# Kernel tuning notes

Hardware: AMD Instinct MI355X
Metric: run time of the kernel (lower is better)

The kernel has to match this reference:

```python
import jax, jax.numpy as jnp
import numpy as np

EMBED_DIM = 1024
N_HEADS = 16
HEAD_DIM = EMBED_DIM // N_HEADS
B, T = 4, 2048


def setup_inputs() -> dict:
    key = jax.random.key(0)
    ks = jax.random.split(key, 5)
    s = 1.0 / np.sqrt(EMBED_DIM)
    return {
        "x": jax.random.normal(ks[0], (B, T, EMBED_DIM), dtype=jnp.float32),
        "w_qkv": jax.random.normal(ks[1], (EMBED_DIM, 3 * EMBED_DIM), dtype=jnp.float32) * s,
        "b_qkv": jnp.zeros((3 * EMBED_DIM,), dtype=jnp.float32),
        "w_out": jax.random.normal(ks[2], (EMBED_DIM, EMBED_DIM), dtype=jnp.float32) * s,
        "b_out": jnp.zeros((EMBED_DIM,), dtype=jnp.float32),
    }


def reference(x, w_qkv, b_qkv, w_out, b_out):
    Bb, Tt, C = x.shape
    qkv = x @ w_qkv + b_qkv                      # (B, T, 3C)
    q, k, v = jnp.split(qkv, 3, axis=-1)
    # (B, H, T, Dh)
    def to_heads(t):
        return t.reshape(Bb, Tt, N_HEADS, HEAD_DIM).transpose(0, 2, 1, 3)
    q, k, v = to_heads(q), to_heads(k), to_heads(v)
    scale = 1.0 / np.sqrt(HEAD_DIM)
    scores = jnp.einsum("bhqd,bhkd->bhqk", q, k) * scale  # (B, H, T, T)
    causal = jnp.tril(jnp.ones((Tt, Tt), dtype=bool))
    scores = jnp.where(causal[None, None], scores, -jnp.inf)
    attn = jax.nn.softmax(scores, axis=-1)
    out = jnp.einsum("bhqk,bhkd->bhqd", attn, v)  # (B, H, T, Dh)
    out = out.transpose(0, 2, 1, 3).reshape(Bb, Tt, C)
    return out @ w_out + b_out
```

## Files before the change

kernel.cpp:

```cpp
#include <hip/hip_runtime.h>

typedef __bf16 bf16;
typedef __bf16 bf16x4 __attribute__((ext_vector_type(4)));
typedef __bf16 bf16x8 __attribute__((ext_vector_type(8)));
typedef float f32x4 __attribute__((ext_vector_type(4)));

#define TSEQ 2048
#define NHEAD 16

__device__ __forceinline__ void gload_lds16(const bf16* g, bf16* s) {
  __builtin_amdgcn_global_load_lds(
      (const __attribute__((address_space(1))) void*)g,
      (__attribute__((address_space(3))) void*)s, 16, 0, 0);
}

__global__ __launch_bounds__(256) void cvt_f32_bf16_kernel(
    const float* __restrict__ in, bf16* __restrict__ out) {
  size_t i = ((size_t)blockIdx.x * 256 + threadIdx.x) * 8;
  float4 v0 = ((const float4*)(in + i))[0];
  float4 v1 = ((const float4*)(in + i))[1];
  bf16x8 o;
  o[0] = (bf16)v0.x; o[1] = (bf16)v0.y; o[2] = (bf16)v0.z; o[3] = (bf16)v0.w;
  o[4] = (bf16)v1.x; o[5] = (bf16)v1.y; o[6] = (bf16)v1.z; o[7] = (bf16)v1.w;
  *(bf16x8*)(out + i) = o;
}

__global__ __launch_bounds__(256) void transpose_cvt_kernel(
    const float* __restrict__ in, bf16* __restrict__ out, int K, int N) {
  __shared__ float tile[32][33];
  int n0 = blockIdx.x * 32, k0 = blockIdx.y * 32;
  int tx = threadIdx.x & 31, ty = threadIdx.x >> 5;
#pragma unroll
  for (int i = ty; i < 32; i += 8)
    tile[i][tx] = in[(size_t)(k0 + i) * N + n0 + tx];
  __syncthreads();
#pragma unroll
  for (int i = ty; i < 32; i += 8)
    out[(size_t)(n0 + i) * K + k0 + tx] = (bf16)tile[tx][i];
}

template <typename OutT>
__global__ __launch_bounds__(256, 2) void gemm_bf16_kernel(
    const bf16* __restrict__ A, const bf16* __restrict__ Bt,
    const float* __restrict__ bias, OutT* __restrict__ C,
    int M, int N, int K, int scale_cols) {
  alignas(16) __shared__ bf16 As[128 * 32];
  alignas(16) __shared__ bf16 Bs[128 * 32];
  const int row0 = blockIdx.y * 128, col0 = blockIdx.x * 128;
  const int tid = threadIdx.x;
  const int wave = tid >> 6, lane = tid & 63;
  const int quad = lane >> 4, lm = lane & 15;
  const int wm = (wave >> 1) * 64, wn = (wave & 1) * 64;

  f32x4 acc[4][4];
  const f32x4 z4 = {0.0f, 0.0f, 0.0f, 0.0f};
#pragma unroll
  for (int i = 0; i < 4; i++)
#pragma unroll
    for (int j = 0; j < 4; j++) acc[i][j] = z4;

  const int sr = tid >> 2, sc = (tid & 3) * 8;
  const bf16* apg = A + (size_t)(row0 + sr) * K + sc;
  const bf16* bpg = Bt + (size_t)(col0 + sr) * K + sc;
  const size_t half = (size_t)64 * K;

  for (int k0 = 0; k0 < K; k0 += 32) {
    __syncthreads();
    gload_lds16(apg, &As[tid * 8]);
    gload_lds16(apg + half, &As[(256 + tid) * 8]);
    gload_lds16(bpg, &Bs[tid * 8]);
    gload_lds16(bpg + half, &Bs[(256 + tid) * 8]);
    apg += 32; bpg += 32;
    __syncthreads();

    bf16x8 af[4], bfr[4];
#pragma unroll
    for (int i = 0; i < 4; i++)
      af[i] = *(const bf16x8*)&As[(wm + i * 16 + lm) * 32 + quad * 8];
#pragma unroll
    for (int j = 0; j < 4; j++)
      bfr[j] = *(const bf16x8*)&Bs[(wn + j * 16 + lm) * 32 + quad * 8];
#pragma unroll
    for (int i = 0; i < 4; i++)
#pragma unroll
      for (int j = 0; j < 4; j++)
        acc[i][j] = __builtin_amdgcn_mfma_f32_16x16x32_bf16(af[i], bfr[j], acc[i][j], 0, 0, 0);
  }

#pragma unroll
  for (int j = 0; j < 4; j++) {
    int gc = col0 + wn + j * 16 + lm;
    float bb = bias[gc];
    float sc2 = (gc < scale_cols) ? 0.125f : 1.0f;
#pragma unroll
    for (int i = 0; i < 4; i++) {
      int gr = row0 + wm + i * 16 + quad * 4;
#pragma unroll
      for (int rr = 0; rr < 4; rr++) {
        float v = (acc[i][j][rr] + bb) * sc2;
        C[(size_t)(gr + rr) * N + gc] = (OutT)v;
      }
    }
  }
}

__global__ __launch_bounds__(256) void transpose_v_kernel(
    const bf16* __restrict__ qkv, bf16* __restrict__ vp) {
  __shared__ bf16 tile[32][33];
  int bh = blockIdx.z, b = bh >> 4, h = bh & 15;
  int t0 = blockIdx.x * 32, d0 = blockIdx.y * 32;
  int tx = threadIdx.x & 31, ty = threadIdx.x >> 5;
#pragma unroll
  for (int i = ty; i < 32; i += 8)
    tile[i][tx] = qkv[(size_t)(b * TSEQ + t0 + i) * 3072 + 2048 + h * 64 + d0 + tx];
  __syncthreads();
#pragma unroll
  for (int i = ty; i < 32; i += 8)
    vp[(size_t)(bh * 64 + d0 + i) * TSEQ + t0 + tx] = tile[tx][i];
}

__global__ __launch_bounds__(256, 4) void flash_attn_kernel(
    const bf16* __restrict__ qkv, const bf16* __restrict__ vp,
    bf16* __restrict__ att) {
  alignas(16) __shared__ bf16 Ks[64 * 72];
  alignas(16) __shared__ bf16 Vts[64 * 72];
  alignas(16) __shared__ bf16 Ps[4][32 * 72];

  const int hb = blockIdx.x;
  const int h = hb & 15, b = hb >> 4;
  const int qt = 15 - blockIdx.y;
  const int q0 = qt * 128;
  const int tid = threadIdx.x;
  const int wave = tid >> 6, lane = tid & 63;
  const int quad = lane >> 4, lm = lane & 15;
  const size_t rowbase = (size_t)b * TSEQ;
  const f32x4 z4 = {0.0f, 0.0f, 0.0f, 0.0f};

  bf16x8 bq[2][2];
#pragma unroll
  for (int nf = 0; nf < 2; nf++)
#pragma unroll
    for (int ks = 0; ks < 2; ks++)
      bq[nf][ks] = *(const bf16x8*)(qkv +
          (rowbase + q0 + wave * 32 + nf * 16 + lm) * 3072 + h * 64 + ks * 32 + quad * 8);

  f32x4 oT[4][2];
#pragma unroll
  for (int mf = 0; mf < 4; mf++)
#pragma unroll
    for (int nf = 0; nf < 2; nf++) oT[mf][nf] = z4;
  float lp[2] = {0.0f, 0.0f};

  const int nkt = 2 * qt + 2;
  const int wrow_lo = q0 + wave * 32;
  const int wrow_hi = wrow_lo + 31;

  for (int kt = 0; kt < nkt; kt++) {
    const int k0 = kt * 64;
    __syncthreads();
    {
      int rr = tid >> 2, c0 = (tid & 3) * 16;
      const float4* ksrc = (const float4*)(qkv + (rowbase + k0 + rr) * 3072 + 1024 + h * 64 + c0);
      float4 ka = ksrc[0], kb = ksrc[1];
      const float4* vsrc = (const float4*)(vp + ((size_t)(b * NHEAD + h) * 64 + rr) * TSEQ + k0 + c0);
      float4 v0 = vsrc[0], v1 = vsrc[1];
      float4* kd = (float4*)&Ks[rr * 72 + c0];
      kd[0] = ka; kd[1] = kb;
      float4* vd = (float4*)&Vts[rr * 72 + c0];
      vd[0] = v0; vd[1] = v1;
    }
    __syncthreads();
    if (k0 > wrow_hi) continue;

    f32x4 s[4][2];
#pragma unroll
    for (int mf = 0; mf < 4; mf++)
#pragma unroll
      for (int nf = 0; nf < 2; nf++) s[mf][nf] = z4;
#pragma unroll
    for (int ks = 0; ks < 2; ks++) {
      bf16x8 ak[4];
#pragma unroll
      for (int mf = 0; mf < 4; mf++)
        ak[mf] = *(const bf16x8*)&Ks[(mf * 16 + lm) * 72 + ks * 32 + quad * 8];
#pragma unroll
      for (int mf = 0; mf < 4; mf++)
#pragma unroll
        for (int nf = 0; nf < 2; nf++)
          s[mf][nf] = __builtin_amdgcn_mfma_f32_16x16x32_bf16(ak[mf], bq[nf][ks], s[mf][nf], 0, 0, 0);
    }

    const bool need_mask = (k0 + 63 > wrow_lo);
#pragma unroll
    for (int nf = 0; nf < 2; nf++) {
      const int qrow = q0 + wave * 32 + nf * 16 + lm;
#pragma unroll
      for (int mf = 0; mf < 4; mf++) {
        bf16x4 pk;
        float psum = 0.0f;
#pragma unroll
        for (int rr = 0; rr < 4; rr++) {
          float pv = __expf(s[mf][nf][rr]);
          if (need_mask) {
            int kv = k0 + mf * 16 + quad * 4 + rr;
            pv = (kv > qrow) ? 0.0f : pv;
          }
          psum += pv;
          pk[rr] = (bf16)pv;
        }
        lp[nf] += psum;
        *(bf16x4*)&Ps[wave][(nf * 16 + lm) * 72 + mf * 16 + quad * 4] = pk;
      }
    }

#pragma unroll
    for (int ks = 0; ks < 2; ks++) {
      bf16x8 av[4], bp[2];
#pragma unroll
      for (int mf = 0; mf < 4; mf++)
        av[mf] = *(const bf16x8*)&Vts[(mf * 16 + lm) * 72 + ks * 32 + quad * 8];
#pragma unroll
      for (int nf = 0; nf < 2; nf++)
        bp[nf] = *(const bf16x8*)&Ps[wave][(nf * 16 + lm) * 72 + ks * 32 + quad * 8];
#pragma unroll
      for (int mf = 0; mf < 4; mf++)
#pragma unroll
        for (int nf = 0; nf < 2; nf++)
          oT[mf][nf] = __builtin_amdgcn_mfma_f32_16x16x32_bf16(av[mf], bp[nf], oT[mf][nf], 0, 0, 0);
    }
  }

  float linv[2];
#pragma unroll
  for (int nf = 0; nf < 2; nf++) {
    float l = lp[nf];
    l += __shfl_xor(l, 16, 64);
    l += __shfl_xor(l, 32, 64);
    linv[nf] = 1.0f / l;
  }

#pragma unroll
  for (int nf = 0; nf < 2; nf++) {
    const size_t grow = rowbase + q0 + wave * 32 + nf * 16 + lm;
#pragma unroll
    for (int mf = 0; mf < 4; mf++) {
      bf16x4 ok;
#pragma unroll
      for (int rr = 0; rr < 4; rr++) ok[rr] = (bf16)(oT[mf][nf][rr] * linv[nf]);
      *(bf16x4*)(att + grow * 1024 + h * 64 + mf * 16 + quad * 4) = ok;
    }
  }
}

extern "C" void kernel_launch(void* const* d_in, const int* in_sizes, int n_in,
                              void* d_out, int out_size, void* d_ws, size_t ws_size,
                              hipStream_t stream) {
  const float* x = (const float*)d_in[0];
  const float* w_qkv = (const float*)d_in[1];
  const float* b_qkv = (const float*)d_in[2];
  const float* w_out = (const float*)d_in[3];
  const float* b_out = (const float*)d_in[4];
  float* out = (float*)d_out;

  char* ws = (char*)d_ws;
  bf16* Xbf   = (bf16*)(ws);
  bf16* Wqkvt = (bf16*)(ws + 16777216);
  bf16* Woutt = (bf16*)(ws + 23068672);
  bf16* QKV   = (bf16*)(ws + 25165824);
  bf16* VP    = (bf16*)(ws + 75497472);
  bf16* ATT   = (bf16*)(ws + 92274688);

  cvt_f32_bf16_kernel<<<4096, 256, 0, stream>>>(x, Xbf);
  transpose_cvt_kernel<<<dim3(96, 32), 256, 0, stream>>>(w_qkv, Wqkvt, 1024, 3072);
  transpose_cvt_kernel<<<dim3(32, 32), 256, 0, stream>>>(w_out, Woutt, 1024, 1024);
  gemm_bf16_kernel<bf16><<<dim3(24, 64), 256, 0, stream>>>(Xbf, Wqkvt, b_qkv, QKV, 8192, 3072, 1024, 1024);
  transpose_v_kernel<<<dim3(64, 2, 64), 256, 0, stream>>>(QKV, VP);
  flash_attn_kernel<<<dim3(64, 16, 1), 256, 0, stream>>>(QKV, VP, ATT);
  gemm_bf16_kernel<float><<<dim3(8, 64), 256, 0, stream>>>(ATT, Woutt, b_out, out, 8192, 1024, 1024, 0);
}
```

Measured before the change: 269.8 us.

## Merge prep kernels, fuse V transpose into QKV GEMM, widen GEMM K-tile with swizzle

Combines the input conversion and both weight transposes into one prep kernel launch. The QKV GEMM epilogue now writes V directly in transposed layout, which removes the separate transpose_v kernel and its extra pass over V. The GEMM uses a 64-wide K tile with an XOR swizzle on LDS reads to cut bank conflicts and halve the number of barrier pairs, and its launch bounds move to 4 blocks per CU. The larger LDS tiles (32KB per block) may limit the occupancy that the new bound asks for.

```diff
diff --git a/kernel.cpp b/kernel.cpp
--- a/kernel.cpp
+++ b/kernel.cpp
@@ -14,22 +14,34 @@
       (__attribute__((address_space(3))) void*)s, 16, 0, 0);
 }
 
-__global__ __launch_bounds__(256) void cvt_f32_bf16_kernel(
-    const float* __restrict__ in, bf16* __restrict__ out) {
-  size_t i = ((size_t)blockIdx.x * 256 + threadIdx.x) * 8;
-  float4 v0 = ((const float4*)(in + i))[0];
-  float4 v1 = ((const float4*)(in + i))[1];
-  bf16x8 o;
-  o[0] = (bf16)v0.x; o[1] = (bf16)v0.y; o[2] = (bf16)v0.z; o[3] = (bf16)v0.w;
-  o[4] = (bf16)v1.x; o[5] = (bf16)v1.y; o[6] = (bf16)v1.z; o[7] = (bf16)v1.w;
-  *(bf16x8*)(out + i) = o;
-}
-
-__global__ __launch_bounds__(256) void transpose_cvt_kernel(
-    const float* __restrict__ in, bf16* __restrict__ out, int K, int N) {
+__global__ __launch_bounds__(256) void prep_kernel(
+    const float* __restrict__ x, bf16* __restrict__ xbf,
+    const float* __restrict__ w_qkv, bf16* __restrict__ wqkvt,
+    const float* __restrict__ w_out, bf16* __restrict__ woutt) {
   __shared__ float tile[32][33];
-  int n0 = blockIdx.x * 32, k0 = blockIdx.y * 32;
-  int tx = threadIdx.x & 31, ty = threadIdx.x >> 5;
+  const int bid = blockIdx.x;
+  const int tid = threadIdx.x;
+  if (bid < 4096) {
+    size_t i = ((size_t)bid * 256 + tid) * 8;
+    float4 v0 = ((const float4*)(x + i))[0];
+    float4 v1 = ((const float4*)(x + i))[1];
+    bf16x8 o;
+    o[0] = (bf16)v0.x; o[1] = (bf16)v0.y; o[2] = (bf16)v0.z; o[3] = (bf16)v0.w;
+    o[4] = (bf16)v1.x; o[5] = (bf16)v1.y; o[6] = (bf16)v1.z; o[7] = (bf16)v1.w;
+    *(bf16x8*)(xbf + i) = o;
+    return;
+  }
+  const float* in; bf16* out; int K, N, n0, k0;
+  if (bid < 7168) {
+    int q = bid - 4096;
+    in = w_qkv; out = wqkvt; K = 1024; N = 3072;
+    n0 = (q % 96) * 32; k0 = (q / 96) * 32;
+  } else {
+    int q = bid - 7168;
+    in = w_out; out = woutt; K = 1024; N = 1024;
+    n0 = (q & 31) * 32; k0 = (q >> 5) * 32;
+  }
+  int tx = tid & 31, ty = tid >> 5;
 #pragma unroll
   for (int i = ty; i < 32; i += 8)
     tile[i][tx] = in[(size_t)(k0 + i) * N + n0 + tx];
@@ -40,12 +52,12 @@
 }
 
 template <typename OutT>
-__global__ __launch_bounds__(256, 2) void gemm_bf16_kernel(
+__global__ __launch_bounds__(256, 4) void gemm_bf16_kernel(
     const bf16* __restrict__ A, const bf16* __restrict__ Bt,
     const float* __restrict__ bias, OutT* __restrict__ C,
-    int M, int N, int K, int scale_cols) {
-  alignas(16) __shared__ bf16 As[128 * 32];
-  alignas(16) __shared__ bf16 Bs[128 * 32];
+    int M, int N, int K, int scale_cols, bf16* __restrict__ vp) {
+  alignas(16) __shared__ bf16 As[128 * 64];
+  alignas(16) __shared__ bf16 Bs[128 * 64];
   const int row0 = blockIdx.y * 128, col0 = blockIdx.x * 128;
   const int tid = threadIdx.x;
   const int wave = tid >> 6, lane = tid & 63;
@@ -59,32 +71,40 @@
 #pragma unroll
     for (int j = 0; j < 4; j++) acc[i][j] = z4;
 
-  const int sr = tid >> 2, sc = (tid & 3) * 8;
-  const bf16* apg = A + (size_t)(row0 + sr) * K + sc;
-  const bf16* bpg = Bt + (size_t)(col0 + sr) * K + sc;
-  const size_t half = (size_t)64 * K;
-
-  for (int k0 = 0; k0 < K; k0 += 32) {
-    __syncthreads();
-    gload_lds16(apg, &As[tid * 8]);
-    gload_lds16(apg + half, &As[(256 + tid) * 8]);
-    gload_lds16(bpg, &Bs[tid * 8]);
-    gload_lds16(bpg + half, &Bs[(256 + tid) * 8]);
-    apg += 32; bpg += 32;
-    __syncthreads();
-
-    bf16x8 af[4], bfr[4];
-#pragma unroll
-    for (int i = 0; i < 4; i++)
-      af[i] = *(const bf16x8*)&As[(wm + i * 16 + lm) * 32 + quad * 8];
-#pragma unroll
-    for (int j = 0; j < 4; j++)
-      bfr[j] = *(const bf16x8*)&Bs[(wn + j * 16 + lm) * 32 + quad * 8];
-#pragma unroll
-    for (int i = 0; i < 4; i++)
+  const int sr0 = tid >> 3;
+  const int js = (tid & 7) ^ ((tid >> 4) & 7);
+  const bf16* apg = A + (size_t)(row0 + sr0) * K + js * 8;
+  const bf16* bpg = Bt + (size_t)(col0 + sr0) * K + js * 8;
+  const size_t row32 = (size_t)32 * K;
+
+  const int sw = (lm >> 1) & 7;
+
+  for (int k0 = 0; k0 < K; k0 += 64) {
+    __syncthreads();
+#pragma unroll
+    for (int p = 0; p < 4; p++) {
+      gload_lds16(apg + p * row32, &As[(p * 256 + tid) * 8]);
+      gload_lds16(bpg + p * row32, &Bs[(p * 256 + tid) * 8]);
+    }
+    apg += 64; bpg += 64;
+    __syncthreads();
+
+#pragma unroll
+    for (int ks = 0; ks < 2; ks++) {
+      const int kc = ((ks * 4 + quad) ^ sw) * 8;
+      bf16x8 af[4], bfr[4];
+#pragma unroll
+      for (int i = 0; i < 4; i++)
+        af[i] = *(const bf16x8*)&As[(wm + i * 16 + lm) * 64 + kc];
 #pragma unroll
       for (int j = 0; j < 4; j++)
-        acc[i][j] = __builtin_amdgcn_mfma_f32_16x16x32_bf16(af[i], bfr[j], acc[i][j], 0, 0, 0);
+        bfr[j] = *(const bf16x8*)&Bs[(wn + j * 16 + lm) * 64 + kc];
+#pragma unroll
+      for (int i = 0; i < 4; i++)
+#pragma unroll
+        for (int j = 0; j < 4; j++)
+          acc[i][j] = __builtin_amdgcn_mfma_f32_16x16x32_bf16(af[i], bfr[j], acc[i][j], 0, 0, 0);
+    }
   }
 
 #pragma unroll
@@ -92,31 +112,30 @@
     int gc = col0 + wn + j * 16 + lm;
     float bb = bias[gc];
     float sc2 = (gc < scale_cols) ? 0.125f : 1.0f;
-#pragma unroll
-    for (int i = 0; i < 4; i++) {
-      int gr = row0 + wm + i * 16 + quad * 4;
-#pragma unroll
-      for (int rr = 0; rr < 4; rr++) {
-        float v = (acc[i][j][rr] + bb) * sc2;
-        C[(size_t)(gr + rr) * N + gc] = (OutT)v;
+    if (vp != nullptr && gc >= 2048) {
+      int gr0 = row0 + wm + quad * 4;
+      int b = gr0 >> 11;
+      size_t vrow = (size_t)(b * 1024 + gc - 2048) * TSEQ;
+#pragma unroll
+      for (int i = 0; i < 4; i++) {
+        int t = (gr0 + i * 16) & (TSEQ - 1);
+        bf16x4 vk;
+#pragma unroll
+        for (int rr = 0; rr < 4; rr++) vk[rr] = (bf16)(acc[i][j][rr] + bb);
+        *(bf16x4*)(vp + vrow + t) = vk;
       }
-    }
-  }
-}
-
-__global__ __launch_bounds__(256) void transpose_v_kernel(
-    const bf16* __restrict__ qkv, bf16* __restrict__ vp) {
-  __shared__ bf16 tile[32][33];
-  int bh = blockIdx.z, b = bh >> 4, h = bh & 15;
-  int t0 = blockIdx.x * 32, d0 = blockIdx.y * 32;
-  int tx = threadIdx.x & 31, ty = threadIdx.x >> 5;
-#pragma unroll
-  for (int i = ty; i < 32; i += 8)
-    tile[i][tx] = qkv[(size_t)(b * TSEQ + t0 + i) * 3072 + 2048 + h * 64 + d0 + tx];
-  __syncthreads();
-#pragma unroll
-  for (int i = ty; i < 32; i += 8)
-    vp[(size_t)(bh * 64 + d0 + i) * TSEQ + t0 + tx] = tile[tx][i];
+    } else {
+#pragma unroll
+      for (int i = 0; i < 4; i++) {
+        int gr = row0 + wm + i * 16 + quad * 4;
+#pragma unroll
+        for (int rr = 0; rr < 4; rr++) {
+          float v = (acc[i][j][rr] + bb) * sc2;
+          C[(size_t)(gr + rr) * N + gc] = (OutT)v;
+        }
+      }
+    }
+  }
 }
 
 __global__ __launch_bounds__(256, 4) void flash_attn_kernel(
@@ -270,11 +289,10 @@
   bf16* VP    = (bf16*)(ws + 75497472);
   bf16* ATT   = (bf16*)(ws + 92274688);
 
-  cvt_f32_bf16_kernel<<<4096, 256, 0, stream>>>(x, Xbf);
-  transpose_cvt_kernel<<<dim3(96, 32), 256, 0, stream>>>(w_qkv, Wqkvt, 1024, 3072);
-  transpose_cvt_kernel<<<dim3(32, 32), 256, 0, stream>>>(w_out, Woutt, 1024, 1024);
-  gemm_bf16_kernel<bf16><<<dim3(24, 64), 256, 0, stream>>>(Xbf, Wqkvt, b_qkv, QKV, 8192, 3072, 1024, 1024);
-  transpose_v_kernel<<<dim3(64, 2, 64), 256, 0, stream>>>(QKV, VP);
+  prep_kernel<<<8192, 256, 0, stream>>>(x, Xbf, w_qkv, Wqkvt, w_out, Woutt);
+  gemm_bf16_kernel<bf16><<<dim3(24, 64), 256, 0, stream>>>(
+      Xbf, Wqkvt, b_qkv, QKV, 8192, 3072, 1024, 1024, VP);
   flash_attn_kernel<<<dim3(64, 16, 1), 256, 0, stream>>>(QKV, VP, ATT);
-  gemm_bf16_kernel<float><<<dim3(8, 64), 256, 0, stream>>>(ATT, Woutt, b_out, out, 8192, 1024, 1024, 0);
-}
+  gemm_bf16_kernel<float><<<dim3(8, 64), 256, 0, stream>>>(
+      ATT, Woutt, b_out, out, 8192, 1024, 1024, 0, nullptr);
+}
```

New measurement: 251.1 us. 6.9% less time.
